# Optimization experiments

Hardware: AMD Instinct MI355X
Metric: run time of the kernel (lower is better)

Reference implementation:

```python
import jax, jax.numpy as jnp
import numpy as np
from jax.scipy.special import gammaln, betainc

B, T, F, H, L = 4096, 40, 1, 128, 2
N_GRID = 100
ALPHA_PIT = 100.0
SQRT_2PI = 2.50662827  # constant used by the torch module


def _gru_layer(x, Wih, Whh, bih, bhh):
    # x: [B, T, Din]; Wih: [3H, Din]; Whh: [3H, H]
    xp = jnp.einsum('btd,gd->btg', x, Wih) + bih  # input projections for all steps
    Hh = Whh.shape[1]

    def step(h, g):
        gh = h @ Whh.T + bhh
        ir, iz, inn = jnp.split(g, 3, axis=-1)
        hr, hz, hn = jnp.split(gh, 3, axis=-1)
        r = jax.nn.sigmoid(ir + hr)
        z = jax.nn.sigmoid(iz + hz)
        n = jnp.tanh(inn + r * hn)
        h_new = (1.0 - z) * n + z * h
        return h_new, h_new

    h0 = jnp.zeros((x.shape[0], Hh), x.dtype)
    hT, seq = jax.lax.scan(step, h0, jnp.swapaxes(xp, 0, 1))
    return jnp.swapaxes(seq, 0, 1), hT  # [B,T,H], [B,H]


def _encoder(x, Wih0, Whh0, bih0, bhh0, Wih1, Whh1, bih1, bhh1):
    s0, h0 = _gru_layer(x, Wih0, Whh0, bih0, bhh0)
    s1, h1 = _gru_layer(s0, Wih1, Whh1, bih1, bhh1)
    # h.transpose(0,1).flatten(1) == concat per-layer final states; pooled = mean over seq of top layer
    return jnp.concatenate([h0, h1, s1.mean(axis=1)], axis=1)  # [B, 3H]


def setup_inputs() -> dict:
    key = jax.random.key(0)
    ks = jax.random.split(key, 32)
    s = 1.0 / np.sqrt(H)  # torch GRU default init scale

    def rn(k, shape, scale=s):
        return (jax.random.normal(k, shape, dtype=jnp.float32) * scale)

    inp = {
        'data_batch': jax.random.normal(ks[0], (B, T, F), dtype=jnp.float32),
        'dX': jax.random.normal(ks[1], (B, F), dtype=jnp.float32) * 0.01,
        'dT': jnp.full((1,), 1.0 / 252.0, dtype=jnp.float32),
    }
    i = 2
    for pfx in ('d_', 's_'):  # drift net, diffusion net
        inp[pfx + 'Wih0'] = rn(ks[i], (3 * H, F)); i += 1
        inp[pfx + 'Whh0'] = rn(ks[i], (3 * H, H)); i += 1
        inp[pfx + 'bih0'] = rn(ks[i], (3 * H,)); i += 1
        inp[pfx + 'bhh0'] = rn(ks[i], (3 * H,)); i += 1
        inp[pfx + 'Wih1'] = rn(ks[i], (3 * H, H)); i += 1
        inp[pfx + 'Whh1'] = rn(ks[i], (3 * H, H)); i += 1
        inp[pfx + 'bih1'] = rn(ks[i], (3 * H,)); i += 1
        inp[pfx + 'bhh1'] = rn(ks[i], (3 * H,)); i += 1
        inp[pfx + 'Wh'] = rn(ks[i], (F, 3 * H)); i += 1
        inp[pfx + 'bh'] = rn(ks[i], (F,)); i += 1
    inp['log_nu'] = jnp.asarray(np.log(4.0), dtype=jnp.float32)
    return inp


def reference(data_batch, dX, dT,
              d_Wih0, d_Whh0, d_bih0, d_bhh0, d_Wih1, d_Whh1, d_bih1, d_bhh1, d_Wh, d_bh,
              s_Wih0, s_Whh0, s_bih0, s_bhh0, s_Wih1, s_Whh1, s_bih1, s_bhh1, s_Wh, s_bh,
              log_nu):
    # drift head: clamp(linear(enc), -20, 20)
    mu = jnp.clip(_encoder(data_batch, d_Wih0, d_Whh0, d_bih0, d_bhh0,
                           d_Wih1, d_Whh1, d_bih1, d_bhh1) @ d_Wh.T + d_bh, -20.0, 20.0)
    # diffusion head: softplus(clamp(...)) + 1e-4
    sigma = jax.nn.softplus(jnp.clip(_encoder(data_batch, s_Wih0, s_Whh0, s_bih0, s_bhh0,
                                              s_Wih1, s_Whh1, s_bih1, s_bhh1) @ s_Wh.T + s_bh,
                                     -20.0, 20.0)) + 1e-4
    df = jnp.clip(jnp.exp(log_nu), 2.1, 30.0)

    loc = mu * dT                      # [B, F]
    scale = sigma * jnp.sqrt(dT)       # [B, F]
    y = (dX - loc) / scale

    # Student-t NLL (matches torch.distributions.StudentT.log_prob)
    lp = (gammaln((df + 1.0) / 2.0) - gammaln(df / 2.0)
          - 0.5 * jnp.log(df * jnp.pi) - jnp.log(scale)
          - (df + 1.0) / 2.0 * jnp.log1p(y * y / df))
    nll = -lp.mean()

    # PIT via Student-t CDF (regularized incomplete beta); nu treated as constant (torch returns None grad for nu)
    dfs = jax.lax.stop_gradient(df)
    xb = dfs / (dfs + y * y)
    ib = betainc(dfs / 2.0, 0.5, xb)
    cdf = jnp.clip(jnp.where(y <= 0.0, 0.5 * ib, 1.0 - 0.5 * ib), 1e-6, 1.0 - 1e-6)  # [B, F]

    # Gaussian-KDE density penalty over a 100-point grid, vectorized across features
    Bn = cdf.shape[0]
    hbw = 1.06 * jax.lax.stop_gradient(jnp.std(cdf, axis=0, ddof=1)) * Bn ** (-0.2) + 1e-5  # [F]
    u = jnp.linspace(0.0, 1.0, N_GRID)
    phi = jnp.exp(-0.5 * ((u[None, None, :] - cdf[:, :, None]) / hbw[None, :, None]) ** 2) / SQRT_2PI
    f_hat = phi.sum(axis=0) / (Bn * hbw[:, None])            # [F, G]
    du = 1.0 / N_GRID
    penalty = (((f_hat - 1.0) ** 2) * du).sum(axis=1).mean()

    return nll + ALPHA_PIT * penalty
```

## Files before the change

### kernel.cpp

```cpp
#include <hip/hip_runtime.h>
#include <math.h>

#define Bn 4096
#define Tn 40
#define Hn 128
#define NGRID 100
#define PI_F 3.14159265358979f
#define SQRT_2PI_F 2.50662827f
#define LOG2E 1.44269504088896f

typedef _Float16 f16;
typedef __attribute__((ext_vector_type(8))) _Float16 f16x8;
typedef __attribute__((ext_vector_type(4))) float f32x4;

struct GruW {
  const f16 *fWhh0, *fWih1, *fWhh1;
  const float *Wih0, *bih0, *bhh0, *bih1, *bhh1, *Wh, *bh;
};
struct WSrc { const float* m[6]; };

__device__ __forceinline__ float rcp_f(float x){ return __builtin_amdgcn_rcpf(x); }
__device__ __forceinline__ float ex2(float x){ return __builtin_amdgcn_exp2f(x); }
__device__ __forceinline__ int swz(int r){
  return ((r&1)<<4) | ((((r>>1)^(r>>3))&1)<<5) | ((r&4)<<4);
}

__global__ __launch_bounds__(256)
void wconv_k(WSrc S, f16* __restrict__ dst)
{
  const int m  = blockIdx.x / 24;
  const int nt = blockIdx.x % 24;
  const int ks = threadIdx.x >> 6;
  const int l  = threadIdx.x & 63;
  const float scale = (nt < 16) ? -LOG2E : (2.0f*LOG2E);
  const float* src = S.m[m] + (size_t)(nt*16 + (l&15))*Hn + ks*32 + (l>>4)*8;
  f16x8 o;
  #pragma unroll
  for (int jj = 0; jj < 8; ++jj) o[jj] = (f16)(src[jj] * scale);
  *((f16x8*)(dst + (size_t)m*49152) + ((nt*4 + ks)*64 + l)) = o;
}

__global__ __launch_bounds__(512, 2)
void gru_mfma(const float* __restrict__ x, GruW Wd, GruW Ws,
              float* __restrict__ mu_out, float* __restrict__ sig_out)
{
  const int net = blockIdx.x >> 7;
  const int r0  = (blockIdx.x & 127) * 32;
  const GruW W  = net ? Ws : Wd;
  const int tid = threadIdx.x;
  const int w   = tid >> 6;
  const int l   = tid & 63;

  __shared__ __align__(16) char smem[131072];
  char* const h0b0 = smem;
  char* const h0b1 = smem + 8192;
  char* const h1b0 = smem + 16384;
  char* const h1b1 = smem + 24576;
  char* const w1iL = smem + 32768;

  {
    const int4* src = (const int4*)W.fWih1;
    int4* dst = (int4*)w1iL;
    #pragma unroll
    for (int k = 0; k < 12; ++k) dst[tid + k*512] = src[tid + k*512];
  }
  ((int4*)h1b1)[tid] = make_int4(0,0,0,0);

  const int j = w*16 + (l & 15);
  const float wr_s = W.Wih0[j]      * (-LOG2E);
  const float wz_s = W.Wih0[Hn+j]   * (-LOG2E);
  const float wn_s = W.Wih0[2*Hn+j] * (2.0f*LOG2E);
  const float br0_s  = (W.bih0[j]      + W.bhh0[j])      * (-LOG2E);
  const float bz0_s  = (W.bih0[Hn+j]   + W.bhh0[Hn+j])   * (-LOG2E);
  const float bin0_s = W.bih0[2*Hn+j] * (2.0f*LOG2E);
  const float bnh0_s = W.bhh0[2*Hn+j] * (2.0f*LOG2E);
  const float br1_s  = (W.bih1[j]      + W.bhh1[j])      * (-LOG2E);
  const float bz1_s  = (W.bih1[Hn+j]   + W.bhh1[Hn+j])   * (-LOG2E);
  const float bin1_s = W.bih1[2*Hn+j] * (2.0f*LOG2E);
  const float bnh1_s = W.bhh1[2*Hn+j] * (2.0f*LOG2E);

  const f16x8* F0  = (const f16x8*)W.fWhh0;
  const f16x8* F1h = (const f16x8*)W.fWhh1;
  f16x8 w0[3][4], w1h[3][4];
  #pragma unroll
  for (int g = 0; g < 3; ++g)
    #pragma unroll
    for (int ks = 0; ks < 4; ++ks) {
      const int idx = ((w + 8*g)*4 + ks)*64 + l;
      w0[g][ks]  = F0[idx];
      w1h[g][ks] = F1h[idx];
    }

  int roff[2][4], woff[2][4];
  {
    const int ra = l & 15, msk = swz(ra);
    #pragma unroll
    for (int mt = 0; mt < 2; ++mt)
      #pragma unroll
      for (int ks = 0; ks < 4; ++ks)
        roff[mt][ks] = (mt*16 + ra)*256 + ((ks*64 + ((l>>4)*16)) ^ msk);
  }
  {
    const int j2 = j*2;
    #pragma unroll
    for (int mt = 0; mt < 2; ++mt)
      #pragma unroll
      for (int q = 0; q < 4; ++q) {
        const int row = mt*16 + (l>>4)*4 + q;
        woff[mt][q] = row*256 + (j2 ^ swz(row & 15));
      }
  }
  int xoff[2][4];
  #pragma unroll
  for (int mt = 0; mt < 2; ++mt)
    #pragma unroll
    for (int q = 0; q < 4; ++q)
      xoff[mt][q] = (r0 + mt*16 + (l>>4)*4 + q)*Tn;

  float h0r[8], h1r[8] = {0,0,0,0,0,0,0,0}, s1r[8] = {0,0,0,0,0,0,0,0};

  __syncthreads();

  #pragma unroll
  for (int mt = 0; mt < 2; ++mt)
    #pragma unroll
    for (int q = 0; q < 4; ++q) {
      const float xv = x[xoff[mt][q] + 0];
      const float rg = rcp_f(1.f + ex2(fmaf(xv, wr_s, br0_s)));
      const float zg = rcp_f(1.f + ex2(fmaf(xv, wz_s, bz0_s)));
      const float xn = fmaf(xv, wn_s, bin0_s);
      const float ng = fmaf(rcp_f(1.f + ex2(fmaf(rg, bnh0_s, xn))), -2.f, 1.f);
      const float hv = fmaf(-zg, ng, ng);
      h0r[mt*4+q] = hv;
      *(f16*)(h0b0 + woff[mt][q]) = (f16)hv;
    }
  __syncthreads();

  for (int i = 0; i < Tn; ++i) {
    const char* h0cur = (i&1) ? h0b1 : h0b0;
    char*       h0nxt = (i&1) ? h0b0 : h0b1;
    const char* h1prv = (i&1) ? h1b0 : h1b1;
    char*       h1cur = (i&1) ? h1b1 : h1b0;

    f32x4 aL0[3][2], aRZ[2][2], aXN[2], aHN[2];
    #pragma unroll
    for (int mt = 0; mt < 2; ++mt) {
      aL0[0][mt] = (f32x4){br0_s,br0_s,br0_s,br0_s};
      aL0[1][mt] = (f32x4){bz0_s,bz0_s,bz0_s,bz0_s};
      aL0[2][mt] = (f32x4){bnh0_s,bnh0_s,bnh0_s,bnh0_s};
      aRZ[0][mt] = (f32x4){br1_s,br1_s,br1_s,br1_s};
      aRZ[1][mt] = (f32x4){bz1_s,bz1_s,bz1_s,bz1_s};
      aXN[mt]    = (f32x4){bin1_s,bin1_s,bin1_s,bin1_s};
      aHN[mt]    = (f32x4){bnh1_s,bnh1_s,bnh1_s,bnh1_s};
    }

    #pragma unroll
    for (int ks = 0; ks < 4; ++ks) {
      const f16x8 a0_0 = *(const f16x8*)(h0cur + roff[0][ks]);
      const f16x8 a0_1 = *(const f16x8*)(h0cur + roff[1][ks]);
      #pragma unroll
      for (int g = 0; g < 3; ++g) {
        const f16x8 bi = *(const f16x8*)(w1iL + (size_t)(((w + 8*g)*4 + ks)*64 + l)*16);
        aL0[g][0] = __builtin_amdgcn_mfma_f32_16x16x32_f16(a0_0, w0[g][ks], aL0[g][0], 0,0,0);
        aL0[g][1] = __builtin_amdgcn_mfma_f32_16x16x32_f16(a0_1, w0[g][ks], aL0[g][1], 0,0,0);
        if (g < 2) {
          aRZ[g][0] = __builtin_amdgcn_mfma_f32_16x16x32_f16(a0_0, bi, aRZ[g][0], 0,0,0);
          aRZ[g][1] = __builtin_amdgcn_mfma_f32_16x16x32_f16(a0_1, bi, aRZ[g][1], 0,0,0);
        } else {
          aXN[0] = __builtin_amdgcn_mfma_f32_16x16x32_f16(a0_0, bi, aXN[0], 0,0,0);
          aXN[1] = __builtin_amdgcn_mfma_f32_16x16x32_f16(a0_1, bi, aXN[1], 0,0,0);
        }
      }
    }
    #pragma unroll
    for (int ks = 0; ks < 4; ++ks) {
      const f16x8 a1_0 = *(const f16x8*)(h1prv + roff[0][ks]);
      const f16x8 a1_1 = *(const f16x8*)(h1prv + roff[1][ks]);
      #pragma unroll
      for (int g = 0; g < 2; ++g) {
        aRZ[g][0] = __builtin_amdgcn_mfma_f32_16x16x32_f16(a1_0, w1h[g][ks], aRZ[g][0], 0,0,0);
        aRZ[g][1] = __builtin_amdgcn_mfma_f32_16x16x32_f16(a1_1, w1h[g][ks], aRZ[g][1], 0,0,0);
      }
      aHN[0] = __builtin_amdgcn_mfma_f32_16x16x32_f16(a1_0, w1h[2][ks], aHN[0], 0,0,0);
      aHN[1] = __builtin_amdgcn_mfma_f32_16x16x32_f16(a1_1, w1h[2][ks], aHN[1], 0,0,0);
    }

    if (i < Tn-1) {
      #pragma unroll
      for (int mt = 0; mt < 2; ++mt)
        #pragma unroll
        for (int q = 0; q < 4; ++q) {
          const int e = mt*4+q;
          const float xv = x[xoff[mt][q] + i + 1];
          const float rg = rcp_f(1.f + ex2(fmaf(xv, wr_s, aL0[0][mt][q])));
          const float zg = rcp_f(1.f + ex2(fmaf(xv, wz_s, aL0[1][mt][q])));
          const float xn = fmaf(xv, wn_s, bin0_s);
          const float ng = fmaf(rcp_f(1.f + ex2(fmaf(rg, aL0[2][mt][q], xn))), -2.f, 1.f);
          const float hv = fmaf(zg, h0r[e] - ng, ng);
          h0r[e] = hv;
          *(f16*)(h0nxt + woff[mt][q]) = (f16)hv;
        }
    }
    #pragma unroll
    for (int mt = 0; mt < 2; ++mt)
      #pragma unroll
      for (int q = 0; q < 4; ++q) {
        const int e = mt*4+q;
        const float rg = rcp_f(1.f + ex2(aRZ[0][mt][q]));
        const float zg = rcp_f(1.f + ex2(aRZ[1][mt][q]));
        const float ng = fmaf(rcp_f(1.f + ex2(fmaf(rg, aHN[mt][q], aXN[mt][q]))), -2.f, 1.f);
        const float hv = fmaf(zg, h1r[e] - ng, ng);
        h1r[e] = hv;
        s1r[e] += hv;
        *(f16*)(h1cur + woff[mt][q]) = (f16)hv;
      }
    __syncthreads();
  }

  const float whA = W.Wh[j], whB = W.Wh[Hn+j], whC = W.Wh[2*Hn+j] * (1.0f/Tn);
  float* hredf = (float*)h0b0;
  #pragma unroll
  for (int mt = 0; mt < 2; ++mt)
    #pragma unroll
    for (int q = 0; q < 4; ++q) {
      const int e = mt*4+q;
      float p = h0r[e]*whA + h1r[e]*whB + s1r[e]*whC;
      p += __shfl_xor(p, 1); p += __shfl_xor(p, 2);
      p += __shfl_xor(p, 4); p += __shfl_xor(p, 8);
      if ((l & 15) == 0) hredf[(mt*16 + (l>>4)*4 + q)*8 + w] = p;
    }
  __syncthreads();
  if (tid < 32) {
    float s = W.bh[0];
    #pragma unroll
    for (int ww = 0; ww < 8; ++ww) s += hredf[tid*8 + ww];
    const float v = fminf(fmaxf(s, -20.f), 20.f);
    const int b = r0 + tid;
    if (net == 0) mu_out[b] = v;
    else          sig_out[b] = log1pf(__expf(v)) + 1e-4f;
  }
}

__device__ float betacf_(float a, float b, float x)
{
  const float FPMIN = 1e-30f, EPS = 3e-7f;
  const float qab = a + b, qap = a + 1.f, qam = a - 1.f;
  float c = 1.f;
  float d = 1.f - qab * x / qap;
  if (fabsf(d) < FPMIN) d = FPMIN;
  d = 1.f / d;
  float h = d;
  for (int m = 1; m <= 100; ++m) {
    const float m2 = 2.f * m;
    float aa = m * (b - m) * x / ((qam + m2) * (a + m2));
    d = 1.f + aa * d; if (fabsf(d) < FPMIN) d = FPMIN;
    c = 1.f + aa / c; if (fabsf(c) < FPMIN) c = FPMIN;
    d = 1.f / d; h *= d * c;
    aa = -(a + m) * (qab + m) * x / ((a + m2) * (qap + m2));
    d = 1.f + aa * d; if (fabsf(d) < FPMIN) d = FPMIN;
    c = 1.f + aa / c; if (fabsf(c) < FPMIN) c = FPMIN;
    d = 1.f / d;
    const float del = d * c; h *= del;
    if (fabsf(del - 1.f) < EPS) break;
  }
  return h;
}

__device__ float betainc_(float a, float b, float x, float cx)
{
  if (x  <= 0.f) return 0.f;
  if (cx <= 0.f) return 1.f;
  const float lx  = (x  > 0.5f) ? log1pf(-cx) : logf(x);
  const float lcx = (cx > 0.5f) ? log1pf(-x)  : logf(cx);
  const float bt = expf(lgammaf(a+b) - lgammaf(a) - lgammaf(b) + a*lx + b*lcx);
  if (x < (a + 1.f) / (a + b + 2.f)) return bt * betacf_(a, b, x) / a;
  else                               return 1.f - bt * betacf_(b, a, cx) / b;
}

__global__ __launch_bounds__(256)
void stats_k(const float* __restrict__ mu, const float* __restrict__ sig,
             const float* __restrict__ dX, const float* __restrict__ dTp,
             const float* __restrict__ log_nu,
             float* __restrict__ cdf_out, float* __restrict__ parts)
{
  const int tid = threadIdx.x;
  const int b = blockIdx.x * 256 + tid;
  const float dT = dTp[0];
  const float df = fminf(fmaxf(expf(log_nu[0]), 2.1f), 30.0f);

  const float m = mu[b], s = sig[b];
  const float scale = s * sqrtf(dT);
  const float y  = (dX[b] - m * dT) / scale;
  const float y2 = y * y;
  const float lp = lgammaf((df + 1.f) * 0.5f) - lgammaf(df * 0.5f)
                 - 0.5f * logf(df * PI_F) - logf(scale)
                 - (df + 1.f) * 0.5f * log1pf(y2 / df);
  const float den = df + y2;
  const float xb = df / den, cxb = y2 / den;
  const float ib = betainc_(0.5f * df, 0.5f, xb, cxb);
  float cdf = (y <= 0.f) ? 0.5f * ib : 1.f - 0.5f * ib;
  cdf = fminf(fmaxf(cdf, 1e-6f), 1.f - 1e-6f);
  cdf_out[b] = cdf;

  __shared__ float red[256];
  red[tid] = lp; __syncthreads();
  for (int o = 128; o > 0; o >>= 1) { if (tid < o) red[tid] += red[tid + o]; __syncthreads(); }
  if (tid == 0) parts[blockIdx.x] = red[0];
  __syncthreads();
  red[tid] = cdf; __syncthreads();
  for (int o = 128; o > 0; o >>= 1) { if (tid < o) red[tid] += red[tid + o]; __syncthreads(); }
  if (tid == 0) parts[16 + blockIdx.x] = red[0];
  __syncthreads();
  red[tid] = cdf * cdf; __syncthreads();
  for (int o = 128; o > 0; o >>= 1) { if (tid < o) red[tid] += red[tid + o]; __syncthreads(); }
  if (tid == 0) parts[32 + blockIdx.x] = red[0];
}

__global__ __launch_bounds__(256)
void kde_k(const float* __restrict__ cdf, const float* __restrict__ parts,
           float* __restrict__ pen)
{
  const int tid = threadIdx.x;
  float sc = 0.f, sc2 = 0.f;
  #pragma unroll
  for (int i = 0; i < 16; ++i) { sc += parts[16+i]; sc2 += parts[32+i]; }
  const float mean = sc / (float)Bn;
  const float var  = (sc2 - (float)Bn * mean * mean) / (float)(Bn - 1);
  const float sd   = sqrtf(fmaxf(var, 0.f));
  const float hbw  = 1.06f * sd * 0.18946457f + 1e-5f;
  const float inv  = 1.0f / hbw;
  const float u    = (float)blockIdx.x / (float)(NGRID - 1);
  const float c    = -0.5f * LOG2E;

  float acc = 0.f;
  for (int k = tid; k < Bn; k += 256) {
    const float d = (u - cdf[k]) * inv;
    acc += ex2(d * d * c);
  }
  __shared__ float sh[256];
  sh[tid] = acc; __syncthreads();
  for (int o = 128; o > 0; o >>= 1) { if (tid < o) sh[tid] += sh[tid + o]; __syncthreads(); }
  if (tid == 0) {
    const float f = sh[0] / (SQRT_2PI_F * (float)Bn * hbw);
    const float dd = f - 1.0f;
    pen[blockIdx.x] = dd * dd * (1.0f / (float)NGRID);
  }
}

__global__ __launch_bounds__(128)
void finish_k(const float* __restrict__ parts, const float* __restrict__ pen,
              float* __restrict__ out)
{
  const int tid = threadIdx.x;
  __shared__ float sh[128];
  sh[tid] = (tid < NGRID) ? pen[tid] : 0.f;
  __syncthreads();
  for (int o = 64; o > 0; o >>= 1) { if (tid < o) sh[tid] += sh[tid + o]; __syncthreads(); }
  if (tid == 0) {
    float slp = 0.f;
    #pragma unroll
    for (int i = 0; i < 16; ++i) slp += parts[i];
    out[0] = (-slp / (float)Bn) + 100.0f * sh[0];
  }
}

extern "C" void kernel_launch(void* const* d_in, const int* in_sizes, int n_in,
                              void* d_out, int out_size, void* d_ws, size_t ws_size,
                              hipStream_t stream)
{
  const float* x      = (const float*)d_in[0];
  const float* dX     = (const float*)d_in[1];
  const float* dT     = (const float*)d_in[2];
  const float* log_nu = (const float*)d_in[23];

  float* w     = (float*)d_ws;
  float* mu    = w;
  float* sig   = w + Bn;
  float* cdf   = w + 2 * Bn;
  float* parts = w + 3 * Bn;
  float* pen   = w + 3 * Bn + 48;
  f16*  fragb  = (f16*)((char*)d_ws + 65536);

  WSrc S;
  S.m[0] = (const float*)d_in[4];
  S.m[1] = (const float*)d_in[7];
  S.m[2] = (const float*)d_in[8];
  S.m[3] = (const float*)d_in[14];
  S.m[4] = (const float*)d_in[17];
  S.m[5] = (const float*)d_in[18];

  GruW Wd { fragb + (size_t)0*49152, fragb + (size_t)1*49152, fragb + (size_t)2*49152,
            (const float*)d_in[3], (const float*)d_in[5], (const float*)d_in[6],
            (const float*)d_in[9], (const float*)d_in[10],
            (const float*)d_in[11], (const float*)d_in[12] };
  GruW Ws { fragb + (size_t)3*49152, fragb + (size_t)4*49152, fragb + (size_t)5*49152,
            (const float*)d_in[13], (const float*)d_in[15], (const float*)d_in[16],
            (const float*)d_in[19], (const float*)d_in[20],
            (const float*)d_in[21], (const float*)d_in[22] };

  wconv_k <<<dim3(6*24), 256, 0, stream>>>(S, fragb);
  gru_mfma<<<dim3(256), 512, 0, stream>>>(x, Wd, Ws, mu, sig);
  stats_k <<<dim3(Bn/256), 256, 0, stream>>>(mu, sig, dX, dT, log_nu, cdf, parts);
  kde_k   <<<dim3(NGRID), 256, 0, stream>>>(cdf, parts, pen);
  finish_k<<<dim3(1), 128, 0, stream>>>(parts, pen, (float*)d_out);
}
```

Before: 131.1 us.

## Keep layer-1 input weights in registers and stage x in LDS

Moves the Wih1 fp16 fragments from shared memory into per-thread registers, which removes the 12 LDS loads per step from the recurrent loop. Each block's slice of the input sequence is preloaded into shared memory once, so the per-step global loads of x go away. Shared memory use falls from 128 KB to 40 KB. Launch bounds drop to one 512-thread block per SM to free registers for the extra 12 f16x8 fragments, trading occupancy for lower per-step LDS traffic and latency.

```diff
diff --git a/kernel.cpp b/kernel.cpp
--- a/kernel.cpp
+++ b/kernel.cpp
@@ -40,7 +40,7 @@
   *((f16x8*)(dst + (size_t)m*49152) + ((nt*4 + ks)*64 + l)) = o;
 }
 
-__global__ __launch_bounds__(512, 2)
+__global__ __launch_bounds__(512, 1)
 void gru_mfma(const float* __restrict__ x, GruW Wd, GruW Ws,
               float* __restrict__ mu_out, float* __restrict__ sig_out)
 {
@@ -51,19 +51,14 @@
   const int w   = tid >> 6;
   const int l   = tid & 63;
 
-  __shared__ __align__(16) char smem[131072];
+  __shared__ __align__(16) char smem[40960];
   char* const h0b0 = smem;
   char* const h0b1 = smem + 8192;
   char* const h1b0 = smem + 16384;
   char* const h1b1 = smem + 24576;
-  char* const w1iL = smem + 32768;
-
-  {
-    const int4* src = (const int4*)W.fWih1;
-    int4* dst = (int4*)w1iL;
-    #pragma unroll
-    for (int k = 0; k < 12; ++k) dst[tid + k*512] = src[tid + k*512];
-  }
+  float* const xall = (float*)(smem + 32768);
+
+  for (int i = tid; i < 32*Tn; i += 512) xall[i] = x[(size_t)r0*Tn + i];
   ((int4*)h1b1)[tid] = make_int4(0,0,0,0);
 
   const int j = w*16 + (l & 15);
@@ -80,14 +75,16 @@
   const float bnh1_s = W.bhh1[2*Hn+j] * (2.0f*LOG2E);
 
   const f16x8* F0  = (const f16x8*)W.fWhh0;
+  const f16x8* F1i = (const f16x8*)W.fWih1;
   const f16x8* F1h = (const f16x8*)W.fWhh1;
-  f16x8 w0[3][4], w1h[3][4];
+  f16x8 w0[3][4], w1i[3][4], w1h[3][4];
   #pragma unroll
   for (int g = 0; g < 3; ++g)
     #pragma unroll
     for (int ks = 0; ks < 4; ++ks) {
       const int idx = ((w + 8*g)*4 + ks)*64 + l;
       w0[g][ks]  = F0[idx];
+      w1i[g][ks] = F1i[idx];
       w1h[g][ks] = F1h[idx];
     }
 
@@ -110,22 +107,17 @@
         woff[mt][q] = row*256 + (j2 ^ swz(row & 15));
       }
   }
-  int xoff[2][4];
+  const int xb = (l>>4)*4*Tn;
+
+  float h0r[8], h1r[8] = {0,0,0,0,0,0,0,0}, s1r[8] = {0,0,0,0,0,0,0,0};
+
+  __syncthreads();
+
   #pragma unroll
   for (int mt = 0; mt < 2; ++mt)
     #pragma unroll
-    for (int q = 0; q < 4; ++q)
-      xoff[mt][q] = (r0 + mt*16 + (l>>4)*4 + q)*Tn;
-
-  float h0r[8], h1r[8] = {0,0,0,0,0,0,0,0}, s1r[8] = {0,0,0,0,0,0,0,0};
-
-  __syncthreads();
-
-  #pragma unroll
-  for (int mt = 0; mt < 2; ++mt)
-    #pragma unroll
     for (int q = 0; q < 4; ++q) {
-      const float xv = x[xoff[mt][q] + 0];
+      const float xv = xall[xb + mt*16*Tn + q*Tn];
       const float rg = rcp_f(1.f + ex2(fmaf(xv, wr_s, br0_s)));
       const float zg = rcp_f(1.f + ex2(fmaf(xv, wz_s, bz0_s)));
       const float xn = fmaf(xv, wn_s, bin0_s);
@@ -160,17 +152,15 @@
       const f16x8 a0_1 = *(const f16x8*)(h0cur + roff[1][ks]);
       #pragma unroll
       for (int g = 0; g < 3; ++g) {
-        const f16x8 bi = *(const f16x8*)(w1iL + (size_t)(((w + 8*g)*4 + ks)*64 + l)*16);
         aL0[g][0] = __builtin_amdgcn_mfma_f32_16x16x32_f16(a0_0, w0[g][ks], aL0[g][0], 0,0,0);
         aL0[g][1] = __builtin_amdgcn_mfma_f32_16x16x32_f16(a0_1, w0[g][ks], aL0[g][1], 0,0,0);
-        if (g < 2) {
-          aRZ[g][0] = __builtin_amdgcn_mfma_f32_16x16x32_f16(a0_0, bi, aRZ[g][0], 0,0,0);
-          aRZ[g][1] = __builtin_amdgcn_mfma_f32_16x16x32_f16(a0_1, bi, aRZ[g][1], 0,0,0);
-        } else {
-          aXN[0] = __builtin_amdgcn_mfma_f32_16x16x32_f16(a0_0, bi, aXN[0], 0,0,0);
-          aXN[1] = __builtin_amdgcn_mfma_f32_16x16x32_f16(a0_1, bi, aXN[1], 0,0,0);
-        }
       }
+      aRZ[0][0] = __builtin_amdgcn_mfma_f32_16x16x32_f16(a0_0, w1i[0][ks], aRZ[0][0], 0,0,0);
+      aRZ[0][1] = __builtin_amdgcn_mfma_f32_16x16x32_f16(a0_1, w1i[0][ks], aRZ[0][1], 0,0,0);
+      aRZ[1][0] = __builtin_amdgcn_mfma_f32_16x16x32_f16(a0_0, w1i[1][ks], aRZ[1][0], 0,0,0);
+      aRZ[1][1] = __builtin_amdgcn_mfma_f32_16x16x32_f16(a0_1, w1i[1][ks], aRZ[1][1], 0,0,0);
+      aXN[0]    = __builtin_amdgcn_mfma_f32_16x16x32_f16(a0_0, w1i[2][ks], aXN[0], 0,0,0);
+      aXN[1]    = __builtin_amdgcn_mfma_f32_16x16x32_f16(a0_1, w1i[2][ks], aXN[1], 0,0,0);
     }
     #pragma unroll
     for (int ks = 0; ks < 4; ++ks) {
@@ -191,7 +181,7 @@
         #pragma unroll
         for (int q = 0; q < 4; ++q) {
           const int e = mt*4+q;
-          const float xv = x[xoff[mt][q] + i + 1];
+          const float xv = xall[xb + mt*16*Tn + q*Tn + i + 1];
           const float rg = rcp_f(1.f + ex2(fmaf(xv, wr_s, aL0[0][mt][q])));
           const float zg = rcp_f(1.f + ex2(fmaf(xv, wz_s, aL0[1][mt][q])));
           const float xn = fmaf(xv, wn_s, bin0_s);
```

New measurement: 170.6 us. +30.1%, slower.
